# Optimization experiments

Measured on AMD Instinct MI355X. Metric: run time of the kernel, lower is better.

Reference implementation:

```python
import jax, jax.numpy as jnp
import numpy as np

# Module hyperparameters (init_kwargs)
NUM_TIME_STEPS = 4
HIDDEN_SIZE = 1024
# LIF dynamics constants
DECAY = 0.9        # membrane leak
THRESHOLD = 1.0    # firing threshold
BETA = 5.0         # surrogate sigmoid sharpness


def setup_inputs() -> dict:
    key = jax.random.key(0)
    k1, k2 = jax.random.split(key)
    B, S, I, H = 32, 128, 64, HIDDEN_SIZE
    x = jax.random.normal(k1, (B, S, I, H), dtype=jnp.float32)
    encoding = jax.random.normal(k2, (I, H), dtype=jnp.float32)
    return {"x": x, "encoding": encoding}


def reference(x, encoding):
    # x: [B, S, I, H], encoding: [I, H]
    B, S, I, H = x.shape
    # i = sum(encoding * x, dim=2) -> [B, S, H]
    drive = jnp.einsum('bsih,ih->bsh', x, encoding)
    # each sequence step is integrated for NUM_TIME_STEPS with the same input
    drive_rep = jnp.repeat(drive, NUM_TIME_STEPS, axis=1)      # [B, S*T, H]
    drive_tbh = jnp.swapaxes(drive_rep, 0, 1)                  # [S*T, B, H]

    def lif_step(v, inp):
        v_new = DECAY * v + inp
        spike = jax.nn.sigmoid(BETA * (v_new - THRESHOLD))     # surrogate spike
        v_reset = v_new - spike * THRESHOLD                    # subtractive reset
        return v_reset, spike

    v0 = jnp.zeros((B, H), dtype=x.dtype)                      # initial_states
    v_final, outputs = jax.lax.scan(lif_step, v0, drive_tbh)   # outputs: [S*T, B, H]
    output_sequence = jnp.swapaxes(outputs, 0, 1)              # [B, S*T, H]
    return output_sequence, v_final
```

## Files before the change

### kernel.cpp

```cpp
#include <hip/hip_runtime.h>
#include <math.h>

#define BB 32
#define SS 128
#define II 64
#define HH 1024
#define TT 4
constexpr float DECAY   = 0.9f;
constexpr float THRESH  = 1.0f;
constexpr float BETA    = 5.0f;

__global__ __launch_bounds__(256) void drive_kernel(
    const float4* __restrict__ x,
    const float4* __restrict__ enc,
    float4* __restrict__ drive)
{
    const int tid = blockIdx.x * blockDim.x + threadIdx.x;
    const int hq  = tid & (HH / 4 - 1);
    const int bs  = tid >> 8;
    const float4* xp = x   + (size_t)bs * II * (HH / 4) + hq;
    const float4* ep = enc + hq;
    float4 acc = make_float4(0.f, 0.f, 0.f, 0.f);
#pragma unroll 8
    for (int i = 0; i < II; ++i) {
        float4 xv = xp[i * (HH / 4)];
        float4 ev = ep[i * (HH / 4)];
        acc.x = fmaf(xv.x, ev.x, acc.x);
        acc.y = fmaf(xv.y, ev.y, acc.y);
        acc.z = fmaf(xv.z, ev.z, acc.z);
        acc.w = fmaf(xv.w, ev.w, acc.w);
    }
    drive[tid] = acc;
}

__global__ __launch_bounds__(64) void lif_kernel(
    const float* __restrict__ drive,
    float* __restrict__ out,
    float* __restrict__ vfinal)
{
    const int tid = blockIdx.x * blockDim.x + threadIdx.x;
    const int h   = tid & (HH - 1);
    const int b   = tid >> 10;
    const float* dp = drive + (size_t)b * SS * HH + h;
    float*       op = out   + (size_t)b * SS * TT * HH + h;

    float v = 0.f;
    float d = dp[0];
    for (int s = 0; s < SS; ++s) {
        float dn = (s + 1 < SS) ? dp[(size_t)(s + 1) * HH] : 0.f;
#pragma unroll
        for (int t = 0; t < TT; ++t) {
            v = fmaf(DECAY, v, d);
            float z  = BETA * (v - THRESH);
            float sp = 1.f / (1.f + expf(-z));
            v -= sp * THRESH;
            op[(size_t)(s * TT + t) * HH] = sp;
        }
        d = dn;
    }
    vfinal[tid] = v;
}

__global__ __launch_bounds__(64) void fused_kernel(
    const float* __restrict__ x,
    const float* __restrict__ enc,
    float* __restrict__ out,
    float* __restrict__ vfinal)
{
    const int tid = blockIdx.x * blockDim.x + threadIdx.x;
    const int h   = tid & (HH - 1);
    const int b   = tid >> 10;
    float e[II];
#pragma unroll
    for (int i = 0; i < II; ++i) e[i] = enc[i * HH + h];

    float* op = out + (size_t)b * SS * TT * HH + h;
    float v = 0.f;
    for (int s = 0; s < SS; ++s) {
        const float* xp = x + ((size_t)(b * SS + s) * II) * HH + h;
        float acc = 0.f;
#pragma unroll
        for (int i = 0; i < II; ++i) acc = fmaf(xp[(size_t)i * HH], e[i], acc);
#pragma unroll
        for (int t = 0; t < TT; ++t) {
            v = fmaf(DECAY, v, acc);
            float z  = BETA * (v - THRESH);
            float sp = 1.f / (1.f + expf(-z));
            v -= sp * THRESH;
            op[(size_t)(s * TT + t) * HH] = sp;
        }
    }
    vfinal[tid] = v;
}

extern "C" void kernel_launch(void* const* d_in, const int* in_sizes, int n_in,
                              void* d_out, int out_size, void* d_ws, size_t ws_size,
                              hipStream_t stream) {
    const float* x   = (const float*)d_in[0];
    const float* enc = (const float*)d_in[1];
    float* out    = (float*)d_out;
    float* vfinal = out + (size_t)BB * SS * TT * HH;

    const size_t drive_bytes = (size_t)BB * SS * HH * sizeof(float);

    if (ws_size >= drive_bytes) {
        float* drive = (float*)d_ws;
        {
            const int n4 = BB * SS * (HH / 4);
            drive_kernel<<<n4 / 256, 256, 0, stream>>>(
                (const float4*)x, (const float4*)enc, (float4*)drive);
        }
        {
            const int n = BB * HH;
            lif_kernel<<<n / 64, 64, 0, stream>>>(drive, out, vfinal);
        }
    } else {
        const int n = BB * HH;
        fused_kernel<<<n / 64, 64, 0, stream>>>(x, enc, out, vfinal);
    }
}
```

Before: 1.420 ms.

## Stage drive in output buffer, batch four sequence rows per thread, fast sigmoid

```diff
diff --git a/kernel.cpp b/kernel.cpp
--- a/kernel.cpp
+++ b/kernel.cpp
@@ -6,89 +6,80 @@
 #define II 64
 #define HH 1024
 #define TT 4
-constexpr float DECAY   = 0.9f;
-constexpr float THRESH  = 1.0f;
-constexpr float BETA    = 5.0f;
+#define HQ (HH / 4)
+
+constexpr float DECAY  = 0.9f;
+constexpr float THRESH = 1.0f;
+constexpr float BETA   = 5.0f;
+
+typedef float f4 __attribute__((ext_vector_type(4)));
 
 __global__ __launch_bounds__(256) void drive_kernel(
-    const float4* __restrict__ x,
-    const float4* __restrict__ enc,
-    float4* __restrict__ drive)
+    const f4* __restrict__ x,
+    const f4* __restrict__ enc,
+    f4* __restrict__ out)
 {
     const int tid = blockIdx.x * blockDim.x + threadIdx.x;
-    const int hq  = tid & (HH / 4 - 1);
-    const int bs  = tid >> 8;
-    const float4* xp = x   + (size_t)bs * II * (HH / 4) + hq;
-    const float4* ep = enc + hq;
-    float4 acc = make_float4(0.f, 0.f, 0.f, 0.f);
-#pragma unroll 8
+    const int hq  = tid & (HQ - 1);
+    const int g   = tid >> 8;
+    const f4* xp = x + ((size_t)g * 4 * II) * HQ + hq;
+    const f4* ep = enc + hq;
+
+    f4 a0 = {0.f, 0.f, 0.f, 0.f};
+    f4 a1 = {0.f, 0.f, 0.f, 0.f};
+    f4 a2 = {0.f, 0.f, 0.f, 0.f};
+    f4 a3 = {0.f, 0.f, 0.f, 0.f};
+
+#pragma unroll 4
     for (int i = 0; i < II; ++i) {
-        float4 xv = xp[i * (HH / 4)];
-        float4 ev = ep[i * (HH / 4)];
-        acc.x = fmaf(xv.x, ev.x, acc.x);
-        acc.y = fmaf(xv.y, ev.y, acc.y);
-        acc.z = fmaf(xv.z, ev.z, acc.z);
-        acc.w = fmaf(xv.w, ev.w, acc.w);
+        f4 ev = ep[(size_t)i * HQ];
+        f4 x0 = __builtin_nontemporal_load(xp + (size_t)i * HQ);
+        f4 x1 = __builtin_nontemporal_load(xp + (size_t)(II + i) * HQ);
+        f4 x2 = __builtin_nontemporal_load(xp + (size_t)(2 * II + i) * HQ);
+        f4 x3 = __builtin_nontemporal_load(xp + (size_t)(3 * II + i) * HQ);
+        a0 = __builtin_elementwise_fma(x0, ev, a0);
+        a1 = __builtin_elementwise_fma(x1, ev, a1);
+        a2 = __builtin_elementwise_fma(x2, ev, a2);
+        a3 = __builtin_elementwise_fma(x3, ev, a3);
     }
-    drive[tid] = acc;
+
+    const int bs = g << 2;
+    const int b  = bs >> 7;
+    const int s0 = bs & (SS - 1);
+    f4* dst = out + ((size_t)b * SS * TT + (size_t)(s0 * TT + 3)) * HQ + hq;
+    dst[0]           = a0;
+    dst[TT * HQ]     = a1;
+    dst[2 * TT * HQ] = a2;
+    dst[3 * TT * HQ] = a3;
 }
 
 __global__ __launch_bounds__(64) void lif_kernel(
-    const float* __restrict__ drive,
     float* __restrict__ out,
     float* __restrict__ vfinal)
 {
     const int tid = blockIdx.x * blockDim.x + threadIdx.x;
     const int h   = tid & (HH - 1);
     const int b   = tid >> 10;
-    const float* dp = drive + (size_t)b * SS * HH + h;
-    float*       op = out   + (size_t)b * SS * TT * HH + h;
+    float* op = out + (size_t)b * SS * TT * HH + h;
 
-    float v = 0.f;
-    float d = dp[0];
+    float v  = 0.f;
+    float d0 = op[(size_t)3 * HH];
+    float d1 = op[(size_t)7 * HH];
+
     for (int s = 0; s < SS; ++s) {
-        float dn = (s + 1 < SS) ? dp[(size_t)(s + 1) * HH] : 0.f;
+        float dn = 0.f;
+        if (s + 2 < SS) dn = op[(size_t)((s + 2) * TT + 3) * HH];
 #pragma unroll
         for (int t = 0; t < TT; ++t) {
-            v = fmaf(DECAY, v, d);
-            float z  = BETA * (v - THRESH);
-            float sp = 1.f / (1.f + expf(-z));
-            v -= sp * THRESH;
+            v = fmaf(DECAY, v, d0);
+            float az = fmaf(-BETA, v, BETA * THRESH);
+            float e  = __expf(az);
+            float sp = __builtin_amdgcn_rcpf(1.f + e);
+            v = fmaf(-THRESH, sp, v);
             op[(size_t)(s * TT + t) * HH] = sp;
         }
-        d = dn;
-    }
-    vfinal[tid] = v;
-}
-
-__global__ __launch_bounds__(64) void fused_kernel(
-    const float* __restrict__ x,
-    const float* __restrict__ enc,
-    float* __restrict__ out,
-    float* __restrict__ vfinal)
-{
-    const int tid = blockIdx.x * blockDim.x + threadIdx.x;
-    const int h   = tid & (HH - 1);
-    const int b   = tid >> 10;
-    float e[II];
-#pragma unroll
-    for (int i = 0; i < II; ++i) e[i] = enc[i * HH + h];
-
-    float* op = out + (size_t)b * SS * TT * HH + h;
-    float v = 0.f;
-    for (int s = 0; s < SS; ++s) {
-        const float* xp = x + ((size_t)(b * SS + s) * II) * HH + h;
-        float acc = 0.f;
-#pragma unroll
-        for (int i = 0; i < II; ++i) acc = fmaf(xp[(size_t)i * HH], e[i], acc);
-#pragma unroll
-        for (int t = 0; t < TT; ++t) {
-            v = fmaf(DECAY, v, acc);
-            float z  = BETA * (v - THRESH);
-            float sp = 1.f / (1.f + expf(-z));
-            v -= sp * THRESH;
-            op[(size_t)(s * TT + t) * HH] = sp;
-        }
+        d0 = d1;
+        d1 = dn;
     }
     vfinal[tid] = v;
 }
@@ -96,26 +87,19 @@
 extern "C" void kernel_launch(void* const* d_in, const int* in_sizes, int n_in,
                               void* d_out, int out_size, void* d_ws, size_t ws_size,
                               hipStream_t stream) {
-    const float* x   = (const float*)d_in[0];
-    const float* enc = (const float*)d_in[1];
+    const f4* x   = (const f4*)d_in[0];
+    const f4* enc = (const f4*)d_in[1];
     float* out    = (float*)d_out;
     float* vfinal = out + (size_t)BB * SS * TT * HH;
 
-    const size_t drive_bytes = (size_t)BB * SS * HH * sizeof(float);
+    (void)d_ws; (void)ws_size;
 
-    if (ws_size >= drive_bytes) {
-        float* drive = (float*)d_ws;
-        {
-            const int n4 = BB * SS * (HH / 4);
-            drive_kernel<<<n4 / 256, 256, 0, stream>>>(
-                (const float4*)x, (const float4*)enc, (float4*)drive);
-        }
-        {
-            const int n = BB * HH;
-            lif_kernel<<<n / 64, 64, 0, stream>>>(drive, out, vfinal);
-        }
-    } else {
+    {
+        const int nthreads = (BB * SS / 4) * HQ;
+        drive_kernel<<<nthreads / 256, 256, 0, stream>>>(x, enc, (f4*)out);
+    }
+    {
         const int n = BB * HH;
-        fused_kernel<<<n / 64, 64, 0, stream>>>(x, enc, out, vfinal);
+        lif_kernel<<<n / 64, 64, 0, stream>>>(out, vfinal);
     }
 }
```

Result: faster. 1.351 ms (-4.8%).
